# Kernel optimization log

Measured on AMD Instinct MI355X. Metric: run time of the kernel, lower is better.

Reference implementation:

```python
import jax, jax.numpy as jnp
import numpy as np

N_NODES = 50000
N_EDGES = 800000
D_FEAT = 128
DIM_H = 128
N_LAYERS = 3
N_CLASSES = 10
N_GRAPHS = 512


def setup_inputs() -> dict:
    key = jax.random.key(0)
    ks = jax.random.split(key, 8)
    x = jax.random.normal(ks[0], (N_NODES, D_FEAT), dtype=jnp.float32)
    W = jax.random.normal(ks[1], (N_LAYERS, DIM_H, DIM_H), dtype=jnp.float32) * 0.1
    b = jnp.zeros((N_LAYERS, DIM_H), dtype=jnp.float32)
    lin_w = jax.random.normal(ks[2], (DIM_H, N_CLASSES), dtype=jnp.float32) * 0.1
    lin_b = jnp.zeros((N_CLASSES,), dtype=jnp.float32)
    edge_index = jax.random.randint(ks[3], (2, N_EDGES), 0, N_NODES, dtype=jnp.int64)
    batch = jnp.sort(jax.random.randint(ks[4], (N_NODES,), 0, N_GRAPHS, dtype=jnp.int64))
    return {"x": x, "W": W, "b": b, "lin_w": lin_w, "lin_b": lin_b,
            "edge_index": edge_index, "batch": batch, "num_layers": N_LAYERS}


def _gcn_norm(edge_index, n_nodes):
    # add self loops (PyG GCNConv default), then symmetric normalization
    loop = jnp.arange(n_nodes, dtype=edge_index.dtype)
    src = jnp.concatenate([edge_index[0], loop])  # [E+N]
    dst = jnp.concatenate([edge_index[1], loop])
    deg = jax.ops.segment_sum(jnp.ones_like(dst, dtype=jnp.float32), dst,
                              num_segments=n_nodes)
    dinv = jnp.where(deg > 0, jax.lax.rsqrt(deg), 0.0)
    norm = dinv[src] * dinv[dst]  # [E+N]
    return src, dst, norm


def _gcn_conv(h, Wi, bi, src, dst, norm, n_nodes):
    h = h @ Wi                       # [N, dim_h] dense GEMM
    msg = h[src] * norm[:, None]     # gather + scale, [E+N, dim_h]
    out = jax.ops.segment_sum(msg, dst, num_segments=n_nodes)  # scatter-add
    return out + bi


def reference(x, W, b, lin_w, lin_b, edge_index, batch, num_layers):
    n_nodes = x.shape[0]
    src, dst, norm = _gcn_norm(edge_index, n_nodes)
    h = x
    for i in range(num_layers):
        h = jax.nn.relu(_gcn_conv(h, W[i], b[i], src, dst, norm, n_nodes))
    # global mean pool over graph ids
    sums = jax.ops.segment_sum(h, batch, num_segments=N_GRAPHS)          # [G, dim_h]
    cnts = jax.ops.segment_sum(jnp.ones((n_nodes,), h.dtype), batch,
                               num_segments=N_GRAPHS)
    hG = sums / jnp.maximum(cnts, 1.0)[:, None]
    # dropout is identity at eval; num_layers > 1 branch applies the linear head
    logits = hG @ lin_w + lin_b
    return hG, jax.nn.log_softmax(logits, axis=1)
```

## Files before the change

### kernel.cpp

```cpp
#include <hip/hip_runtime.h>
#include <hip/hip_bf16.h>
#include <hip/hip_fp8.h>

#define NN 50000
#define NE 800000
#define FD 128
#define NG 512
#define NC 10
#define NL 3
#define CAP 64
#define GEMM_B 782
#define COMP_B 910
#define NBIN 196
#define BCAP 4800
#define CHUNK 4096
#define NCHUNK 196
#define PART_B (NCHUNK + COMP_B)
#define PATCH_B 12500

typedef unsigned short u16;
typedef unsigned char u8;
typedef unsigned int u32;
typedef short bf16x8 __attribute__((ext_vector_type(8)));
typedef float f32x4 __attribute__((ext_vector_type(4)));
typedef float f32x2 __attribute__((ext_vector_type(2)));

__device__ __forceinline__ float b2f(u16 v) {
    union { u32 u; float f; } c; c.u = ((u32)v) << 16; return c.f;
}
__device__ __forceinline__ u16 f2b(float f) {
    __hip_bfloat16 h = __float2bfloat16(f);
    return *(u16*)&h;
}
__device__ __forceinline__ float p2f(u8 b) {
    __hip_fp8_e4m3 h; h.__x = b; return (float)h;
}
__device__ __forceinline__ u8 f2p(float f) {
    __hip_fp8_e4m3 h(f); return h.__x;
}

#if defined(__has_builtin)
#if __has_builtin(__builtin_amdgcn_cvt_pk_f32_fp8)
#define HAVE_PKCVT 1
#endif
#endif
template<bool HI>
__device__ __forceinline__ f32x2 pkcvt(u32 u) {
#ifdef HAVE_PKCVT
    return __builtin_amdgcn_cvt_pk_f32_fp8((int)u, HI);
#else
    f32x2 r;
    r[0] = p2f((u8)(HI ? (u >> 16) : u));
    r[1] = p2f((u8)(HI ? (u >> 24) : (u >> 8)));
    return r;
#endif
}

__global__ __launch_bounds__(256) void k_part(const int* __restrict__ src,
                                              const int* __restrict__ dst,
                                              int* __restrict__ gcnt,
                                              int* __restrict__ ebuf,
                                              const float* __restrict__ W,
                                              u16* __restrict__ wt,
                                              const float* __restrict__ x,
                                              u8* __restrict__ Bout) {
    __shared__ int stage[CHUNK];
    __shared__ int hist[NBIN];
    __shared__ int lbase[NBIN];
    __shared__ int gbase[NBIN];
    __shared__ int scan[256];
    const int bid = blockIdx.x;
    const int tid = threadIdx.x;
    if (bid >= NCHUNK) {
        const int q = bid - NCHUNK;
        if (q < GEMM_B) {
            const int wid = q * 4 + (tid >> 6);
            if (wid >= 3125) return;
            const int row0 = wid * 16;
            const int lane = tid & 63;
            const int m = lane & 15;
            const int qq = lane >> 4;
            f32x4 acc[8];
#pragma unroll
            for (int ct = 0; ct < 8; ++ct) acc[ct] = (f32x4){0.f, 0.f, 0.f, 0.f};
            const float* arow = x + (size_t)(row0 + m) * FD + qq * 8;
            const float* wbase = W + (size_t)qq * 8 * FD + m;
#pragma unroll
            for (int kb = 0; kb < 4; ++kb) {
                const float4 p0 = *(const float4*)(arow + kb * 32);
                const float4 p1 = *(const float4*)(arow + kb * 32 + 4);
                bf16x8 af;
                af[0] = (short)f2b(p0.x); af[1] = (short)f2b(p0.y);
                af[2] = (short)f2b(p0.z); af[3] = (short)f2b(p0.w);
                af[4] = (short)f2b(p1.x); af[5] = (short)f2b(p1.y);
                af[6] = (short)f2b(p1.z); af[7] = (short)f2b(p1.w);
#pragma unroll
                for (int ct = 0; ct < 8; ++ct) {
                    const float* wp = wbase + (size_t)kb * 32 * FD + ct * 16;
                    bf16x8 bf;
#pragma unroll
                    for (int j = 0; j < 8; ++j)
                        bf[j] = (short)f2b(wp[(size_t)j * FD]);
                    acc[ct] = __builtin_amdgcn_mfma_f32_16x16x32_bf16(af, bf,
                                                                      acc[ct], 0, 0, 0);
                }
            }
#pragma unroll
            for (int ct = 0; ct < 8; ++ct)
#pragma unroll
                for (int r = 0; r < 4; ++r)
                    Bout[(size_t)(row0 + qq * 4 + r) * FD + ct * 16 + m] =
                        f2p(acc[ct][r]);
        } else {
            const int c = (q - GEMM_B) * 256 + tid + FD * FD;
            const int l = c >> 14, rr = c & 16383, k = rr >> 7, n = rr & 127;
            wt[(l << 14) + n * FD + k] = f2b(W[c]);
        }
        return;
    }
    if (tid < NBIN) hist[tid] = 0;
    __syncthreads();
    const int e00 = bid * CHUNK;
    int dv[16], sv[16], pp[16];
#pragma unroll
    for (int k = 0; k < 4; ++k) {
        const int e = e00 + k * 1024 + tid * 4;
        if (e < NE) {
            const int4 d4 = *(const int4*)(dst + e);
            const int4 s4 = *(const int4*)(src + e);
            dv[k*4+0] = d4.x; dv[k*4+1] = d4.y; dv[k*4+2] = d4.z; dv[k*4+3] = d4.w;
            sv[k*4+0] = s4.x; sv[k*4+1] = s4.y; sv[k*4+2] = s4.z; sv[k*4+3] = s4.w;
        } else {
            dv[k*4+0] = dv[k*4+1] = dv[k*4+2] = dv[k*4+3] = -1;
        }
    }
#pragma unroll
    for (int k = 0; k < 16; ++k)
        if (dv[k] >= 0) pp[k] = atomicAdd(&hist[((u32)dv[k]) >> 8], 1);
    __syncthreads();
    const int hv = (tid < NBIN) ? hist[tid] : 0;
    scan[tid] = hv;
    __syncthreads();
    for (int o = 1; o < 256; o <<= 1) {
        const int t = (tid >= o) ? scan[tid - o] : 0;
        __syncthreads();
        scan[tid] += t;
        __syncthreads();
    }
    if (tid < NBIN) {
        lbase[tid] = scan[tid] - hv;
        gbase[tid] = atomicAdd(&gcnt[tid], hv);
    }
    const int total = scan[255];
    __syncthreads();
#pragma unroll
    for (int k = 0; k < 16; ++k)
        if (dv[k] >= 0)
            stage[lbase[((u32)dv[k]) >> 8] + pp[k]] = (dv[k] << 16) | sv[k];
    __syncthreads();
    for (int i = tid; i < total; i += 256) {
        const int pv = stage[i];
        const int b = ((u32)pv) >> 24;
        const int idx = gbase[b] + (i - lbase[b]);
        if (idx < BCAP) ebuf[(size_t)b * BCAP + idx] = pv;
    }
}

__global__ __launch_bounds__(256) void k_build(const int* __restrict__ gcnt,
                                               const int* __restrict__ ebuf,
                                               int* __restrict__ cnt,
                                               int* __restrict__ bkt) {
    __shared__ int cl[256];
    __shared__ int bl[256 * CAP];
    const int b = blockIdx.x;
    const int tid = threadIdx.x;
    cl[tid] = 0;
    __syncthreads();
    const int m = min(gcnt[b], BCAP);
    const int* eb = ebuf + (size_t)b * BCAP;
    for (int i = tid; i < m; i += 256) {
        const int pv = eb[i];
        const int ld = (((u32)pv) >> 16) & 255;
        const int slot = atomicAdd(&cl[ld], 1);
        if (slot < CAP) bl[ld * CAP + slot] = pv & 0xFFFF;
    }
    __syncthreads();
    const int n0 = b * 256;
    const int nh = min(256, NN - n0);
    if (tid < nh) cnt[n0 + tid] = cl[tid];
    int4* dstp = (int4*)(bkt + (size_t)n0 * CAP);
    const int4* srcp = (const int4*)bl;
    const int ti = nh * (CAP / 4);
    for (int i = tid; i < ti; i += 256) dstp[i] = srcp[i];
}

__global__ __launch_bounds__(256) void k_patch(const int* __restrict__ cnt,
                                               int* __restrict__ bkt) {
    const int i = blockIdx.x * 256 + threadIdx.x;
    const int d = i >> 6;
    const int s = i & 63;
    if (s < cnt[d]) {
        const int v = bkt[i];
        const u32 w = (u32)f2b(rsqrtf((float)(cnt[v] + 1)));
        bkt[i] = (int)(((u32)v & 0xFFFFu) | (w << 16));
    }
}

template<bool W8>
__device__ __forceinline__ float4 gather_node(const int rs, const int re,
                                              const int* __restrict__ bkt,
                                              const u8* __restrict__ B,
                                              const float di, const int n,
                                              const float4 bb, const int f) {
    const u32 us = *(const u32*)(B + (size_t)n * FD + f);
    f32x2 aL0 = {0.f, 0.f}, aL1 = {0.f, 0.f}, aL2 = {0.f, 0.f}, aL3 = {0.f, 0.f};
    f32x2 aH0 = {0.f, 0.f}, aH1 = {0.f, 0.f}, aH2 = {0.f, 0.f}, aH3 = {0.f, 0.f};
    int e = rs;
    if (W8) {
        for (; e + 8 <= re; e += 8) {
            const int4 p0 = *(const int4*)(bkt + e);
            const int4 p1 = *(const int4*)(bkt + e + 4);
            const u32 r0 = *(const u32*)(B + (size_t)(p0.x & 0xFFFF) * FD + f);
            const u32 r1 = *(const u32*)(B + (size_t)(p0.y & 0xFFFF) * FD + f);
            const u32 r2 = *(const u32*)(B + (size_t)(p0.z & 0xFFFF) * FD + f);
            const u32 r3 = *(const u32*)(B + (size_t)(p0.w & 0xFFFF) * FD + f);
            const u32 r4 = *(const u32*)(B + (size_t)(p1.x & 0xFFFF) * FD + f);
            const u32 r5 = *(const u32*)(B + (size_t)(p1.y & 0xFFFF) * FD + f);
            const u32 r6 = *(const u32*)(B + (size_t)(p1.z & 0xFFFF) * FD + f);
            const u32 r7 = *(const u32*)(B + (size_t)(p1.w & 0xFFFF) * FD + f);
            const float w0 = b2f((u16)((u32)p0.x >> 16));
            const float w1 = b2f((u16)((u32)p0.y >> 16));
            const float w2 = b2f((u16)((u32)p0.z >> 16));
            const float w3 = b2f((u16)((u32)p0.w >> 16));
            const float w4 = b2f((u16)((u32)p1.x >> 16));
            const float w5 = b2f((u16)((u32)p1.y >> 16));
            const float w6 = b2f((u16)((u32)p1.z >> 16));
            const float w7 = b2f((u16)((u32)p1.w >> 16));
            aL0 += pkcvt<false>(r0) * w0; aH0 += pkcvt<true>(r0) * w0;
            aL1 += pkcvt<false>(r1) * w1; aH1 += pkcvt<true>(r1) * w1;
            aL2 += pkcvt<false>(r2) * w2; aH2 += pkcvt<true>(r2) * w2;
            aL3 += pkcvt<false>(r3) * w3; aH3 += pkcvt<true>(r3) * w3;
            aL0 += pkcvt<false>(r4) * w4; aH0 += pkcvt<true>(r4) * w4;
            aL1 += pkcvt<false>(r5) * w5; aH1 += pkcvt<true>(r5) * w5;
            aL2 += pkcvt<false>(r6) * w6; aH2 += pkcvt<true>(r6) * w6;
            aL3 += pkcvt<false>(r7) * w7; aH3 += pkcvt<true>(r7) * w7;
        }
    }
    for (; e + 4 <= re; e += 4) {
        const int4 p0 = *(const int4*)(bkt + e);
        const u32 r0 = *(const u32*)(B + (size_t)(p0.x & 0xFFFF) * FD + f);
        const u32 r1 = *(const u32*)(B + (size_t)(p0.y & 0xFFFF) * FD + f);
        const u32 r2 = *(const u32*)(B + (size_t)(p0.z & 0xFFFF) * FD + f);
        const u32 r3 = *(const u32*)(B + (size_t)(p0.w & 0xFFFF) * FD + f);
        const float w0 = b2f((u16)((u32)p0.x >> 16));
        const float w1 = b2f((u16)((u32)p0.y >> 16));
        const float w2 = b2f((u16)((u32)p0.z >> 16));
        const float w3 = b2f((u16)((u32)p0.w >> 16));
        aL0 += pkcvt<false>(r0) * w0; aH0 += pkcvt<true>(r0) * w0;
        aL1 += pkcvt<false>(r1) * w1; aH1 += pkcvt<true>(r1) * w1;
        aL2 += pkcvt<false>(r2) * w2; aH2 += pkcvt<true>(r2) * w2;
        aL3 += pkcvt<false>(r3) * w3; aH3 += pkcvt<true>(r3) * w3;
    }
    for (; e < re; ++e) {
        const int pk = bkt[e];
        const u32 r0 = *(const u32*)(B + (size_t)(pk & 0xFFFF) * FD + f);
        const float w0 = b2f((u16)((u32)pk >> 16));
        aL0 += pkcvt<false>(r0) * w0; aH0 += pkcvt<true>(r0) * w0;
    }
    aL0 += pkcvt<false>(us) * di;
    aH0 += pkcvt<true>(us) * di;
    const f32x2 L = (aL0 + aL1) + (aL2 + aL3);
    const f32x2 H = (aH0 + aH1) + (aH2 + aH3);
    float4 r;
    r.x = fmaxf(fmaf(L[0], di, bb.x), 0.f);
    r.y = fmaxf(fmaf(L[1], di, bb.y), 0.f);
    r.z = fmaxf(fmaf(H[0], di, bb.z), 0.f);
    r.w = fmaxf(fmaf(H[1], di, bb.w), 0.f);
    return r;
}

__global__ __launch_bounds__(512) void k_gg(const int* __restrict__ cnt,
                                            const int* __restrict__ bkt,
                                            const u8* __restrict__ Bin,
                                            const float* __restrict__ bias,
                                            const u16* __restrict__ WTn,
                                            u8* __restrict__ Bout) {
    __shared__ u16 sA[16][FD + 8];
    const int tid = threadIdx.x;
    const int wave = tid >> 6;
    const int lane = tid & 63;
    const int nb = blockIdx.x * 16;
    {
        const int half = lane >> 5;
        const int n = nb + wave * 2 + half;
        const int f = (lane & 31) * 4;
        const int cn = cnt[n];
        const int rs = n * CAP;
        const float di = rsqrtf((float)(cn + 1));
        const float4 bb = *(const float4*)(bias + f);
        const float4 r = gather_node<true>(rs, rs + cn, bkt, Bin, di, n, bb, f);
        ushort4 o;
        o.x = f2b(r.x); o.y = f2b(r.y); o.z = f2b(r.z); o.w = f2b(r.w);
        *(ushort4*)&sA[wave * 2 + half][f] = o;
    }
    __syncthreads();
    const int ct = wave;
    const int m = lane & 15;
    const int q = lane >> 4;
    f32x4 acc = (f32x4){0.f, 0.f, 0.f, 0.f};
    const u16* wrow = WTn + (size_t)m * FD + q * 8 + (size_t)ct * 16 * FD;
#pragma unroll
    for (int kb = 0; kb < 4; ++kb) {
        bf16x8 af = *(const bf16x8*)&sA[m][q * 8 + kb * 32];
        bf16x8 bf = *(const bf16x8*)(wrow + kb * 32);
        acc = __builtin_amdgcn_mfma_f32_16x16x32_bf16(af, bf, acc, 0, 0, 0);
    }
#pragma unroll
    for (int r = 0; r < 4; ++r)
        Bout[(size_t)(nb + q * 4 + r) * FD + ct * 16 + m] = f2p(acc[r]);
}

__global__ __launch_bounds__(1024) void k_gpool(const int* __restrict__ cnt,
                                                const int* __restrict__ bkt,
                                                const u8* __restrict__ B,
                                                const float* __restrict__ bias,
                                                const int* __restrict__ batch,
                                                const float* __restrict__ lin_w,
                                                const float* __restrict__ lin_b,
                                                float* __restrict__ out) {
    __shared__ float sfeat[32][FD + 4];
    __shared__ float hm[FD];
    __shared__ int bnd[2];
    __shared__ float part2[2 * NC];
    const int g = blockIdx.x;
    const int tid = threadIdx.x;
    const int lane = tid & 63;
    const int slot = (tid >> 6) * 2 + (lane >> 5);
    const int f = (lane & 31) * 4;
    if (tid < 2) {
        const int key = g + tid;
        int lo = 0, hi = NN;
        while (lo < hi) {
            const int mid = (lo + hi) >> 1;
            if (batch[mid] < key) lo = mid + 1; else hi = mid;
        }
        bnd[tid] = lo;
    }
    __syncthreads();
    const int r0 = bnd[0], r1 = bnd[1];
    const float4 bb = *(const float4*)(bias + f);
    float s0 = 0.f, s1 = 0.f, s2 = 0.f, s3 = 0.f;
    for (int r = r0 + slot; r < r1; r += 32) {
        const int cn = cnt[r];
        const int rs = r * CAP;
        const float di = rsqrtf((float)(cn + 1));
        const float4 v = gather_node<false>(rs, rs + cn, bkt, B, di, r, bb, f);
        s0 += v.x; s1 += v.y; s2 += v.z; s3 += v.w;
    }
    sfeat[slot][f] = s0;
    sfeat[slot][f + 1] = s1;
    sfeat[slot][f + 2] = s2;
    sfeat[slot][f + 3] = s3;
    __syncthreads();
    if (tid < 128) {
        float tot = 0.f;
#pragma unroll
        for (int s = 0; s < 32; ++s) tot += sfeat[s][tid];
        const float mean = tot / fmaxf((float)(r1 - r0), 1.0f);
        hm[tid] = mean;
        out[(size_t)g * FD + tid] = mean;
    }
    __syncthreads();
    if (tid < 128) {
        const float hv = hm[tid];
        const int wv = tid >> 6;
#pragma unroll
        for (int c = 0; c < NC; ++c) {
            float p = hv * lin_w[tid * NC + c];
#pragma unroll
            for (int o = 32; o > 0; o >>= 1) p += __shfl_down(p, o, 64);
            if ((tid & 63) == 0) part2[c * 2 + wv] = p;
        }
    }
    __syncthreads();
    if (tid == 0) {
        float lg[NC];
        float m = -1e30f;
#pragma unroll
        for (int c = 0; c < NC; ++c) {
            lg[c] = part2[2 * c] + part2[2 * c + 1] + lin_b[c];
            m = fmaxf(m, lg[c]);
        }
        float s = 0.f;
#pragma unroll
        for (int c = 0; c < NC; ++c) s += expf(lg[c] - m);
        const float lse = m + logf(s);
        float* o = out + (size_t)NG * FD + (size_t)g * NC;
#pragma unroll
        for (int c = 0; c < NC; ++c) o[c] = lg[c] - lse;
    }
}

extern "C" void kernel_launch(void* const* d_in, const int* in_sizes, int n_in,
                              void* d_out, int out_size, void* d_ws, size_t ws_size,
                              hipStream_t stream) {
    const float* x     = (const float*)d_in[0];
    const float* W     = (const float*)d_in[1];
    const float* bias  = (const float*)d_in[2];
    const float* lin_w = (const float*)d_in[3];
    const float* lin_b = (const float*)d_in[4];
    const int*   src   = (const int*)d_in[5];
    const int*   dst   = src + NE;
    const int*   batch = (const int*)d_in[6];

    u8*    B0     = (u8*)d_ws;
    u8*    B1     = B0 + (size_t)NN * FD;
    u16*   WT     = (u16*)(B1 + (size_t)NN * FD);
    int*   bkt    = (int*)(WT + (size_t)NL * FD * FD);
    int*   cnt    = bkt + (size_t)NN * CAP;
    int*   gcnt   = cnt + NN;
    int*   ebuf   = (int*)B1;
    float* out    = (float*)d_out;

    (void)hipMemsetAsync(gcnt, 0, NBIN * sizeof(int), stream);
    k_part<<<PART_B, 256, 0, stream>>>(src, dst, gcnt, ebuf, W, WT, x, B0);
    k_build<<<NBIN, 256, 0, stream>>>(gcnt, ebuf, cnt, bkt);
    k_patch<<<PATCH_B, 256, 0, stream>>>(cnt, bkt);

    k_gg<<<NN / 16, 512, 0, stream>>>(cnt, bkt, B0, bias,
                                      WT + (size_t)1 * FD * FD, B1);
    k_gg<<<NN / 16, 512, 0, stream>>>(cnt, bkt, B1, bias + FD,
                                      WT + (size_t)2 * FD * FD, B0);
    k_gpool<<<NG, 1024, 0, stream>>>(cnt, bkt, B0, bias + 2 * FD,
                                     batch, lin_w, lin_b, out);
}
```

Before: 213.3 us.

## Stage transposed bf16 weights in LDS for first GEMM, widen build, switch pool gather

The first-layer GEMM blocks now convert W to bf16 once into a padded, transposed LDS tile and read B fragments as 16-byte vectors. Before, each lane did strided scalar global loads and conversions per MFMA. The partition kernel's shared arrays are aliased into the same LDS buffer. k_build now runs with 512 threads per block, and the pooling kernel switches gather_node to the W8 template variant. The LDS staging adds a per-block weight-transpose prologue and a larger LDS footprint, which could reduce occupancy of k_part.

```diff
diff --git a/kernel.cpp b/kernel.cpp
--- a/kernel.cpp
+++ b/kernel.cpp
@@ -17,6 +17,7 @@
 #define NCHUNK 196
 #define PART_B (NCHUNK + COMP_B)
 #define PATCH_B 12500
+#define WLD 136
 
 typedef unsigned short u16;
 typedef unsigned char u8;
@@ -64,16 +65,18 @@
                                               u16* __restrict__ wt,
                                               const float* __restrict__ x,
                                               u8* __restrict__ Bout) {
-    __shared__ int stage[CHUNK];
-    __shared__ int hist[NBIN];
-    __shared__ int lbase[NBIN];
-    __shared__ int gbase[NBIN];
-    __shared__ int scan[256];
+    __shared__ __align__(16) u32 smem[(FD * WLD) / 2];
     const int bid = blockIdx.x;
     const int tid = threadIdx.x;
     if (bid >= NCHUNK) {
         const int q = bid - NCHUNK;
         if (q < GEMM_B) {
+            u16* swt = (u16*)smem;
+            for (int i = tid; i < FD * FD; i += 256) {
+                const int k = i >> 7, n = i & 127;
+                swt[n * WLD + k] = f2b(W[i]);
+            }
+            __syncthreads();
             const int wid = q * 4 + (tid >> 6);
             if (wid >= 3125) return;
             const int row0 = wid * 16;
@@ -84,7 +87,6 @@
 #pragma unroll
             for (int ct = 0; ct < 8; ++ct) acc[ct] = (f32x4){0.f, 0.f, 0.f, 0.f};
             const float* arow = x + (size_t)(row0 + m) * FD + qq * 8;
-            const float* wbase = W + (size_t)qq * 8 * FD + m;
 #pragma unroll
             for (int kb = 0; kb < 4; ++kb) {
                 const float4 p0 = *(const float4*)(arow + kb * 32);
@@ -96,11 +98,8 @@
                 af[6] = (short)f2b(p1.z); af[7] = (short)f2b(p1.w);
 #pragma unroll
                 for (int ct = 0; ct < 8; ++ct) {
-                    const float* wp = wbase + (size_t)kb * 32 * FD + ct * 16;
-                    bf16x8 bf;
-#pragma unroll
-                    for (int j = 0; j < 8; ++j)
-                        bf[j] = (short)f2b(wp[(size_t)j * FD]);
+                    const bf16x8 bf = *(const bf16x8*)
+                        &swt[(ct * 16 + m) * WLD + qq * 8 + kb * 32];
                     acc[ct] = __builtin_amdgcn_mfma_f32_16x16x32_bf16(af, bf,
                                                                       acc[ct], 0, 0, 0);
                 }
@@ -118,6 +117,11 @@
         }
         return;
     }
+    int* stage = (int*)smem;
+    int* hist  = (int*)smem + CHUNK;
+    int* lbase = hist + NBIN;
+    int* gbase = lbase + NBIN;
+    int* scan  = gbase + NBIN;
     if (tid < NBIN) hist[tid] = 0;
     __syncthreads();
     const int e00 = bid * CHUNK;
@@ -166,7 +170,7 @@
     }
 }
 
-__global__ __launch_bounds__(256) void k_build(const int* __restrict__ gcnt,
+__global__ __launch_bounds__(512) void k_build(const int* __restrict__ gcnt,
                                                const int* __restrict__ ebuf,
                                                int* __restrict__ cnt,
                                                int* __restrict__ bkt) {
@@ -174,11 +178,11 @@
     __shared__ int bl[256 * CAP];
     const int b = blockIdx.x;
     const int tid = threadIdx.x;
-    cl[tid] = 0;
+    if (tid < 256) cl[tid] = 0;
     __syncthreads();
     const int m = min(gcnt[b], BCAP);
     const int* eb = ebuf + (size_t)b * BCAP;
-    for (int i = tid; i < m; i += 256) {
+    for (int i = tid; i < m; i += 512) {
         const int pv = eb[i];
         const int ld = (((u32)pv) >> 16) & 255;
         const int slot = atomicAdd(&cl[ld], 1);
@@ -191,7 +195,7 @@
     int4* dstp = (int4*)(bkt + (size_t)n0 * CAP);
     const int4* srcp = (const int4*)bl;
     const int ti = nh * (CAP / 4);
-    for (int i = tid; i < ti; i += 256) dstp[i] = srcp[i];
+    for (int i = tid; i < ti; i += 512) dstp[i] = srcp[i];
 }
 
 __global__ __launch_bounds__(256) void k_patch(const int* __restrict__ cnt,
@@ -354,7 +358,7 @@
         const int cn = cnt[r];
         const int rs = r * CAP;
         const float di = rsqrtf((float)(cn + 1));
-        const float4 v = gather_node<false>(rs, rs + cn, bkt, B, di, r, bb, f);
+        const float4 v = gather_node<true>(rs, rs + cn, bkt, B, di, r, bb, f);
         s0 += v.x; s1 += v.y; s2 += v.z; s3 += v.w;
     }
     sfeat[slot][f] = s0;
@@ -424,7 +428,7 @@
 
     (void)hipMemsetAsync(gcnt, 0, NBIN * sizeof(int), stream);
     k_part<<<PART_B, 256, 0, stream>>>(src, dst, gcnt, ebuf, W, WT, x, B0);
-    k_build<<<NBIN, 256, 0, stream>>>(gcnt, ebuf, cnt, bkt);
+    k_build<<<NBIN, 512, 0, stream>>>(gcnt, ebuf, cnt, bkt);
     k_patch<<<PATCH_B, 256, 0, stream>>>(cnt, bkt);
 
     k_gg<<<NN / 16, 512, 0, stream>>>(cnt, bkt, B0, bias,
```

Result: slower. 221.7 us (+3.9%).
